# Kernel optimization log

Measured on AMD Instinct MI355X. Metric: run time of the kernel, lower is better.

The kernel has to match this reference:

```python
import math
import jax, jax.numpy as jnp
import numpy as np

B, L, C_S, C_Z, H, C, PQK, PV = 1, 768, 256, 128, 8, 32, 4, 8
OUT_DIM = H * C + H * PV * 3 + H * PV + H * 4  # 544
EPS_LN = 1e-5


def _ln(x, w, b):
    m = jnp.mean(x, axis=-1, keepdims=True)
    v = jnp.mean((x - m) ** 2, axis=-1, keepdims=True)
    return (x - m) * jax.lax.rsqrt(v + EPS_LN) * w + b


def setup_inputs() -> dict:
    key = jax.random.key(0)
    ks = jax.random.split(key, 16)
    f = lambda k, shape, s=1.0: jax.random.normal(k, shape, jnp.float32) * s
    w = 0.05  # weight init scale
    return {
        "s": f(ks[0], (B, L, C_S)),
        "z": f(ks[1], (B, L, L, C_Z)),
        "R": f(ks[2], (B, L, 3, 3)),
        "t": f(ks[3], (B, L, 3)),
        "mask": jnp.ones((B, L), jnp.float32),
        "ln_s_w": jnp.ones((C_S,), jnp.float32),
        "ln_s_b": jnp.zeros((C_S,), jnp.float32),
        "ln_z_w": jnp.ones((C_Z,), jnp.float32),
        "ln_z_b": jnp.zeros((C_Z,), jnp.float32),
        "Wq": f(ks[4], (C_S, H * C), w),
        "Wk": f(ks[5], (C_S, H * C), w),
        "Wv": f(ks[6], (C_S, H * C), w),
        "W_pair_bias": f(ks[7], (C_Z, H), w),
        "Wq_pts": f(ks[8], (C_S, H * PQK * 3), w),
        "Wk_pts": f(ks[9], (C_S, H * PQK * 3), w),
        "Wv_pts": f(ks[10], (C_S, H * PV * 3), w),
        "point_weights": f(ks[11], (H,), 0.1),
        "W_pair_out": f(ks[12], (C_Z, H * 4), w),
        "W_out": f(ks[13], (OUT_DIM, C_S), w),
        "b_out": jnp.zeros((C_S,), jnp.float32),
    }


def reference(s, z, R, t, mask, ln_s_w, ln_s_b, ln_z_w, ln_z_b,
              Wq, Wk, Wv, W_pair_bias, Wq_pts, Wk_pts, Wv_pts,
              point_weights, W_pair_out, W_out, b_out):
    s = _ln(s, ln_s_w, ln_s_b)               # [B,L,c_s]
    z = _ln(z, ln_z_w, ln_z_b)               # [B,L,L,c_z]

    q = (s @ Wq).reshape(B, L, H, C)
    k = (s @ Wk).reshape(B, L, H, C)
    v = (s @ Wv).reshape(B, L, H, C)

    scalar_logits = jnp.einsum('bihc,bjhc->bhij', q, k) / math.sqrt(C)
    pair_bias = jnp.transpose(z @ W_pair_bias, (0, 3, 1, 2))  # [B,H,L,L]

    q_pts = (s @ Wq_pts).reshape(B, L, H, PQK, 3)
    k_pts = (s @ Wk_pts).reshape(B, L, H, PQK, 3)
    v_pts = (s @ Wv_pts).reshape(B, L, H, PV, 3)

    t_b = t[:, :, None, None, :]
    apply_T = lambda p: jnp.einsum('blxy,blhpy->blhpx', R, p) + t_b
    q_pts_g = apply_T(q_pts)  # [B,L,H,Pqk,3]
    k_pts_g = apply_T(k_pts)
    v_pts_g = apply_T(v_pts)  # [B,L,H,Pv,3]

    diff = q_pts_g[:, :, None] - k_pts_g[:, None]          # [B,L,L,H,P,3]
    sq_dist = jnp.sum(diff ** 2, axis=(-1, -2))            # [B,L,L,H]
    sq_dist = jnp.transpose(sq_dist, (0, 3, 1, 2))         # [B,H,L,L]

    pw = jax.nn.softplus(point_weights)[None, :, None, None]
    logits = scalar_logits + pair_bias - 0.5 * pw * sq_dist

    pair_mask = mask[:, :, None] * mask[:, None, :]
    logits = jnp.where(pair_mask[:, None] == 0, -1e9, logits)
    attn = jax.nn.softmax(logits, axis=-1)                 # [B,H,L,L]

    scalar_out = jnp.einsum('bhij,bjhc->bihc', attn, v).reshape(B, L, H * C)

    pair_v = (z @ W_pair_out).reshape(B, L, L, H, 4)
    pair_out = jnp.einsum('bhij,bijhd->bihd', attn, pair_v).reshape(B, L, H * 4)

    pt_out_g = jnp.einsum('bhij,bjhpc->bihpc', attn, v_pts_g)    # [B,L,H,Pv,3]
    # invert transform: R^T (x - t)
    pt_out_l = jnp.einsum('blxy,blhpx->blhpy', R, pt_out_g - t_b)
    point_out = pt_out_l.reshape(B, L, H * PV * 3)
    point_norms = jnp.sqrt(jnp.sum(pt_out_l ** 2, axis=-1) + 1e-8).reshape(B, L, H * PV)

    s_update = jnp.concatenate([scalar_out, point_out, point_norms, pair_out], axis=-1)
    s_update = s_update @ W_out + b_out
    s_update = s_update * mask[:, :, None]
    return s_update, attn
```

## Files before the change

kernel.cpp:

```cpp
#include <hip/hip_runtime.h>
#include <math.h>

#define L 768
#define CS 256
#define CZ 128
#define H 8
#define LL (L*L)

typedef __attribute__((ext_vector_type(8))) short bf16x8;
typedef __attribute__((ext_vector_type(4))) float floatx4;

static __device__ __forceinline__ unsigned short f2bf(float f){
  unsigned int u = __float_as_uint(f);
  unsigned int r = (u + 0x7fffu + ((u >> 16) & 1u)) >> 16;
  return (unsigned short)r;
}
static __device__ __forceinline__ float bf2f(unsigned short u){
  return __uint_as_float(((unsigned int)u) << 16);
}

__global__ void k_ln_s(const float* __restrict__ s, const float* __restrict__ w,
                       const float* __restrict__ b, float* __restrict__ out) {
  int i = blockIdx.x, t = threadIdx.x;
  __shared__ float red[256];
  float x = s[i*CS + t];
  red[t] = x; __syncthreads();
  for (int s2=128; s2>0; s2>>=1){ if (t<s2) red[t]+=red[t+s2]; __syncthreads(); }
  float mean = red[0] * (1.0f/CS); __syncthreads();
  float d = x - mean;
  red[t] = d*d; __syncthreads();
  for (int s2=128; s2>0; s2>>=1){ if (t<s2) red[t]+=red[t+s2]; __syncthreads(); }
  float var = red[0] * (1.0f/CS);
  float rstd = rsqrtf(var + 1e-5f);
  out[i*CS+t] = d*rstd*w[t] + b[t];
}

__global__ void k_proj(const float* __restrict__ s_n,
                       const float* __restrict__ Wq, const float* __restrict__ Wk, const float* __restrict__ Wv,
                       const float* __restrict__ Wqp, const float* __restrict__ Wkp, const float* __restrict__ Wvp,
                       const float* __restrict__ R, const float* __restrict__ t,
                       float* __restrict__ q, float* __restrict__ kT, float* __restrict__ v,
                       float* __restrict__ qpg, float* __restrict__ kpgT, float* __restrict__ vpg) {
  int i0 = blockIdx.x*2, tid = threadIdx.x;
  __shared__ float srow[2][256];
  __shared__ float qraw[2][96], kraw[2][96], vraw[2][192];
  __shared__ float Rl[2][9], tl[2][3];
  srow[0][tid] = s_n[i0*CS + tid];
  srow[1][tid] = s_n[(i0+1)*CS + tid];
  if (tid < 18) Rl[tid/9][tid%9] = R[i0*9 + tid];
  if (tid >= 24 && tid < 30) tl[(tid-24)/3][(tid-24)%3] = t[i0*3 + (tid-24)];
  __syncthreads();
  float aq0=0.f, ak0=0.f, av0=0.f, aq1=0.f, ak1=0.f, av1=0.f;
  #pragma unroll 4
  for (int c=0;c<256;c++){
    float s0=srow[0][c], s1=srow[1][c];
    float wq=Wq[c*256+tid], wk=Wk[c*256+tid], wv=Wv[c*256+tid];
    aq0=fmaf(s0,wq,aq0); aq1=fmaf(s1,wq,aq1);
    ak0=fmaf(s0,wk,ak0); ak1=fmaf(s1,wk,ak1);
    av0=fmaf(s0,wv,av0); av1=fmaf(s1,wv,av1);
  }
  q[i0*256+tid]=aq0; q[(i0+1)*256+tid]=aq1;
  kT[(size_t)tid*L + i0]=ak0; kT[(size_t)tid*L + i0+1]=ak1;
  v[i0*256+tid]=av0; v[(i0+1)*256+tid]=av1;
  if (tid < 96){
    float a10=0.f,a20=0.f,a11=0.f,a21=0.f;
    #pragma unroll 4
    for (int c=0;c<256;c++){
      float s0=srow[0][c], s1=srow[1][c];
      float w1=Wqp[c*96+tid], w2=Wkp[c*96+tid];
      a10=fmaf(s0,w1,a10); a11=fmaf(s1,w1,a11);
      a20=fmaf(s0,w2,a20); a21=fmaf(s1,w2,a21);
    }
    qraw[0][tid]=a10; qraw[1][tid]=a11; kraw[0][tid]=a20; kraw[1][tid]=a21;
  }
  if (tid < 192){
    float a30=0.f,a31=0.f;
    #pragma unroll 4
    for (int c=0;c<256;c++){
      float w3=Wvp[c*192+tid];
      a30=fmaf(srow[0][c],w3,a30); a31=fmaf(srow[1][c],w3,a31);
    }
    vraw[0][tid]=a30; vraw[1][tid]=a31;
  }
  __syncthreads();
  #pragma unroll
  for (int rr=0; rr<2; rr++){
    int i = i0 + rr;
    if (tid < 32){
      int b0 = tid*3;
      float px=qraw[rr][b0], py=qraw[rr][b0+1], pz=qraw[rr][b0+2];
      #pragma unroll
      for (int x=0;x<3;x++)
        qpg[i*96 + b0 + x] = Rl[rr][x*3]*px + Rl[rr][x*3+1]*py + Rl[rr][x*3+2]*pz + tl[rr][x];
    } else if (tid < 64){
      int b0 = (tid-32)*3;
      float px=kraw[rr][b0], py=kraw[rr][b0+1], pz=kraw[rr][b0+2];
      #pragma unroll
      for (int x=0;x<3;x++)
        kpgT[(size_t)(b0+x)*L + i] = Rl[rr][x*3]*px + Rl[rr][x*3+1]*py + Rl[rr][x*3+2]*pz + tl[rr][x];
    } else if (tid < 128){
      int b0 = (tid-64)*3;
      float px=vraw[rr][b0], py=vraw[rr][b0+1], pz=vraw[rr][b0+2];
      #pragma unroll
      for (int x=0;x<3;x++)
        vpg[i*192 + b0 + x] = Rl[rr][x*3]*px + Rl[rr][x*3+1]*py + Rl[rr][x*3+2]*pz + tl[rr][x];
    }
  }
}

__global__ void k_prep(const float* __restrict__ lzw, const float* __restrict__ lzb,
                       const float* __restrict__ Wpb, const float* __restrict__ Wpo,
                       unsigned short* __restrict__ Bpack, float* __restrict__ uv) {
  int tid = threadIdx.x, bx = blockIdx.x;
  if (bx == 0){
    if (tid < 48){
      int o = tid;
      float uo = 0.f, vo = 0.f;
      for (int c=0;c<128;c++){
        float W = (o<8) ? Wpb[c*8+o] : ((o<40) ? Wpo[c*32+o-8] : 0.f);
        uo = fmaf(lzw[c], W, uo);
        vo = fmaf(lzb[c], W, vo);
      }
      uv[o] = uo; uv[48+o] = vo;
    }
    return;
  }
  int idx = (bx-1)*256 + tid;
  int jj = idx & 7, lane = (idx>>3)&63, kb = (idx>>9)&3, nt = idx>>11;
  int c = kb*32 + (lane>>4)*8 + jj;
  int o = nt*16 + (lane&15);
  float W = (o<8) ? Wpb[c*8+o] : ((o<40) ? Wpo[c*32+o-8] : 0.f);
  Bpack[idx] = f2bf(lzw[c]*W);
}

__global__ __launch_bounds__(256) void k_zfuse(
    const float* __restrict__ z, const unsigned short* __restrict__ Bpack,
    const float* __restrict__ uv, float* __restrict__ pb, unsigned short* __restrict__ pvb) {
  int i = blockIdx.x, jt = blockIdx.y, tid = threadIdx.x;
  int j0 = jt * 128;
  __shared__ unsigned short znb[128*136];
  __shared__ float smean[128], srstd[128];

  int lane = tid & 63;
  const bf16x8* Bp = (const bf16x8*)Bpack;
  bf16x8 bfr[3][4];
  #pragma unroll
  for (int nt=0; nt<3; nt++)
    #pragma unroll
    for (int kb=0; kb<4; kb++)
      bfr[nt][kb] = Bp[(nt*4+kb)*64 + lane];

  int row = tid >> 1, sub = tid & 1;
  const float4* zrow = (const float4*)(z + ((size_t)i*L + j0 + row)*CZ);
  float sm = 0.f, sq = 0.f;
  #pragma unroll 8
  for (int kk=0; kk<16; kk++){
    float4 v4 = zrow[sub + 2*kk];
    sm += (v4.x+v4.y)+(v4.z+v4.w);
    sq = fmaf(v4.x,v4.x, fmaf(v4.y,v4.y, fmaf(v4.z,v4.z, fmaf(v4.w,v4.w, sq))));
    ushort4 pk = make_ushort4(f2bf(v4.x), f2bf(v4.y), f2bf(v4.z), f2bf(v4.w));
    *(ushort4*)&znb[row*136 + (sub+2*kk)*4] = pk;
  }
  sm += __shfl_xor(sm,1); sq += __shfl_xor(sq,1);
  if (sub == 0){
    float mean = sm*(1.f/128.f);
    float var  = sq*(1.f/128.f) - mean*mean;
    smean[row] = mean; srstd[row] = rsqrtf(var + 1e-5f);
  }

  int w = tid >> 6;
  int n16 = lane & 15, quad = lane >> 4;
  #pragma unroll
  for (int mt2=0; mt2<2; mt2++){
    int mt = w*2 + mt2;
    floatx4 acc0 = {0,0,0,0}, acc1 = {0,0,0,0}, acc2 = {0,0,0,0};
    #pragma unroll
    for (int kb=0; kb<4; kb++){
      bf16x8 afrag = *(const bf16x8*)&znb[(mt*16 + n16)*136 + kb*32 + quad*8];
      acc0 = __builtin_amdgcn_mfma_f32_16x16x32_bf16(afrag, bfr[0][kb], acc0, 0,0,0);
      acc1 = __builtin_amdgcn_mfma_f32_16x16x32_bf16(afrag, bfr[1][kb], acc1, 0,0,0);
      acc2 = __builtin_amdgcn_mfma_f32_16x16x32_bf16(afrag, bfr[2][kb], acc2, 0,0,0);
    }
    #pragma unroll
    for (int nt=0; nt<3; nt++){
      int o = nt*16 + n16;
      if (o >= 40) continue;
      float uo = uv[o], vo = uv[48+o];
      const floatx4 acc = (nt==0) ? acc0 : (nt==1) ? acc1 : acc2;
      #pragma unroll
      for (int reg=0; reg<4; reg++){
        int jl = mt*16 + quad*4 + reg;
        int j = j0 + jl;
        float val = srstd[jl]*(acc[reg] - smean[jl]*uo) + vo;
        if (o < 8) pb[(size_t)o*LL + (size_t)i*L + j] = val;
        else {
          int oo = o - 8;
          pvb[(size_t)(oo>>2)*LL*4 + ((size_t)i*L + j)*4 + (oo&3)] = f2bf(val);
        }
      }
    }
  }
}

__global__ __launch_bounds__(256) void k_attn3(
    const float* __restrict__ q, const float* __restrict__ kT, const float* __restrict__ v,
    const float* __restrict__ qpg, const float* __restrict__ kpgT, const float* __restrict__ vpg,
    float* __restrict__ attn, const unsigned short* __restrict__ pvb,
    const float* __restrict__ R, const float* __restrict__ t,
    const float* __restrict__ point_weights, const float* __restrict__ mask,
    float* __restrict__ su) {
  const int h   = blockIdx.y;
  const int tid = threadIdx.x;
  const int il  = tid >> 5;
  const int i   = blockIdx.x*8 + il;
  const int jg  = tid & 31;

  __shared__ float sml[8][768];
  __shared__ float sptg[8][24];
  __shared__ float sptl[8][24];

  const float pw = log1pf(__expf(point_weights[h]));
  const float mi = mask[i];

  float qreg[32];
  {
    const float4* qr = (const float4*)(q + (size_t)i*256 + h*32);
    #pragma unroll
    for (int c4=0;c4<8;c4++){
      float4 t4 = qr[c4];
      qreg[c4*4+0]=t4.x; qreg[c4*4+1]=t4.y; qreg[c4*4+2]=t4.z; qreg[c4*4+3]=t4.w;
    }
  }
  float qp[12];
  {
    const float4* qr = (const float4*)(qpg + (size_t)i*96 + h*12);
    #pragma unroll
    for (int c4=0;c4<3;c4++){
      float4 t4 = qr[c4];
      qp[c4*4+0]=t4.x; qp[c4*4+1]=t4.y; qp[c4*4+2]=t4.z; qp[c4*4+3]=t4.w;
    }
  }

  const float* kbase  = kT   + (size_t)(h*32)*L + jg*4;
  const float* kpbase = kpgT + (size_t)(h*12)*L + jg*4;
  float* pbrow = attn + (size_t)h*LL + (size_t)i*L + jg*4;

  float lgr[24];
  #pragma unroll
  for (int jt=0; jt<6; jt++){
    const int j0 = jt*128;
    float d0=0.f,d1=0.f,d2=0.f,d3=0.f;
    #pragma unroll
    for (int c=0;c<32;c++){
      float4 kv = *(const float4*)(kbase + (size_t)c*L + j0);
      float qc = qreg[c];
      d0 = fmaf(qc, kv.x, d0); d1 = fmaf(qc, kv.y, d1);
      d2 = fmaf(qc, kv.z, d2); d3 = fmaf(qc, kv.w, d3);
    }
    float s0=0.f,s1=0.f,s2=0.f,s3=0.f;
    #pragma unroll
    for (int pc=0;pc<12;pc++){
      float4 kv = *(const float4*)(kpbase + (size_t)pc*L + j0);
      float qc = qp[pc];
      float e0=qc-kv.x, e1=qc-kv.y, e2=qc-kv.z, e3=qc-kv.w;
      s0=fmaf(e0,e0,s0); s1=fmaf(e1,e1,s1); s2=fmaf(e2,e2,s2); s3=fmaf(e3,e3,s3);
    }
    float4 pb4 = *(const float4*)(pbrow + j0);
    float4 mk4 = *(const float4*)(mask + j0 + jg*4);
    const float SCL = 0.17677669529663687f;
    float l0 = fmaf(d0,SCL,pb4.x) - 0.5f*pw*s0;
    float l1 = fmaf(d1,SCL,pb4.y) - 0.5f*pw*s1;
    float l2 = fmaf(d2,SCL,pb4.z) - 0.5f*pw*s2;
    float l3 = fmaf(d3,SCL,pb4.w) - 0.5f*pw*s3;
    if (mi*mk4.x == 0.f) l0 = -1e9f;
    if (mi*mk4.y == 0.f) l1 = -1e9f;
    if (mi*mk4.z == 0.f) l2 = -1e9f;
    if (mi*mk4.w == 0.f) l3 = -1e9f;
    lgr[jt*4+0]=l0; lgr[jt*4+1]=l1; lgr[jt*4+2]=l2; lgr[jt*4+3]=l3;
  }

  float m = -1e30f;
  #pragma unroll
  for (int u=0;u<24;u++) m = fmaxf(m, lgr[u]);
  #pragma unroll
  for (int d=1; d<32; d<<=1) m = fmaxf(m, __shfl_xor(m, d));
  float ss = 0.f;
  #pragma unroll
  for (int u=0;u<24;u++){ float e = __expf(lgr[u]-m); lgr[u]=e; ss+=e; }
  #pragma unroll
  for (int d=1; d<32; d<<=1) ss += __shfl_xor(ss, d);
  float inv = 1.0f/ss;
  #pragma unroll
  for (int u=0;u<24;u++) lgr[u] *= inv;
  #pragma unroll
  for (int jt=0;jt<6;jt++){
    float4 a4;
    a4.x=lgr[jt*4+0]; a4.y=lgr[jt*4+1]; a4.z=lgr[jt*4+2]; a4.w=lgr[jt*4+3];
    *(float4*)&sml[il][jt*128 + jg*4] = a4;
    *(float4*)(pbrow + jt*128) = a4;
  }
  __syncthreads();

  {
    const float* vp = v + h*32 + jg;
    const float* aw = sml[il];
    float a0=0.f,a1=0.f,a2=0.f,a3=0.f;
    for (int j=0;j<768;j+=4){
      float4 w4 = *(const float4*)&aw[j];
      a0 = fmaf(w4.x, vp[(j+0)*256], a0);
      a1 = fmaf(w4.y, vp[(j+1)*256], a1);
      a2 = fmaf(w4.z, vp[(j+2)*256], a2);
      a3 = fmaf(w4.w, vp[(j+3)*256], a3);
    }
    su[(size_t)i*544 + h*32 + jg] = (a0+a1)+(a2+a3);
  }

  if (tid < 192){
    int i2 = tid/24, e = tid - i2*24;
    const float* pp = vpg + h*24 + e;
    const float* aw = sml[i2];
    float a0=0.f,a1=0.f,a2=0.f,a3=0.f;
    for (int j=0;j<768;j+=4){
      float4 w4 = *(const float4*)&aw[j];
      a0 = fmaf(w4.x, pp[(j+0)*192], a0);
      a1 = fmaf(w4.y, pp[(j+1)*192], a1);
      a2 = fmaf(w4.z, pp[(j+2)*192], a2);
      a3 = fmaf(w4.w, pp[(j+3)*192], a3);
    }
    sptg[i2][e] = (a0+a1)+(a2+a3);
  } else if (tid < 224){
    int qq = tid-192; int i2 = qq>>2, d = qq&3;
    int ii = blockIdx.x*8 + i2;
    const unsigned short* bp = pvb + (size_t)h*LL*4 + (size_t)ii*L*4 + d;
    const float* aw = sml[i2];
    float a0=0.f,a1=0.f,a2=0.f,a3=0.f;
    for (int j=0;j<768;j+=4){
      float4 w4 = *(const float4*)&aw[j];
      a0 = fmaf(w4.x, bf2f(bp[(j+0)*4]), a0);
      a1 = fmaf(w4.y, bf2f(bp[(j+1)*4]), a1);
      a2 = fmaf(w4.z, bf2f(bp[(j+2)*4]), a2);
      a3 = fmaf(w4.w, bf2f(bp[(j+3)*4]), a3);
    }
    su[(size_t)ii*544 + 512 + h*4 + d] = (a0+a1)+(a2+a3);
  }
  __syncthreads();

  if (tid < 192){
    int i2 = tid/24, rem = tid - i2*24, p = rem/3, y = rem - p*3;
    int ii = blockIdx.x*8 + i2;
    float acc = 0.f;
    #pragma unroll
    for (int x=0;x<3;x++)
      acc = fmaf(R[ii*9 + x*3 + y], sptg[i2][p*3+x] - t[ii*3+x], acc);
    sptl[i2][rem] = acc;
    su[(size_t)ii*544 + 256 + h*24 + rem] = acc;
  }
  __syncthreads();

  if (tid < 64){
    int i2 = tid>>3, p = tid&7;
    int ii = blockIdx.x*8 + i2;
    float x0=sptl[i2][p*3], x1=sptl[i2][p*3+1], x2=sptl[i2][p*3+2];
    su[(size_t)ii*544 + 448 + h*8 + p] = sqrtf(x0*x0+x1*x1+x2*x2 + 1e-8f);
  }
}

__global__ void k_out(const float* __restrict__ su_pre, const float* __restrict__ W_out,
                      const float* __restrict__ b_out, const float* __restrict__ mask,
                      float* __restrict__ out) {
  int i = blockIdx.x, tid = threadIdx.x;
  __shared__ float srow[544];
  for (int idx=tid; idx<544; idx+=256) srow[idx] = su_pre[i*544+idx];
  __syncthreads();
  float acc = b_out[tid];
  #pragma unroll 4
  for (int c=0;c<544;c++) acc = fmaf(srow[c], W_out[c*256+tid], acc);
  out[i*256+tid] = acc * mask[i];
}

extern "C" void kernel_launch(void* const* d_in, const int* in_sizes, int n_in,
                              void* d_out, int out_size, void* d_ws, size_t ws_size,
                              hipStream_t stream) {
  const float* s    = (const float*)d_in[0];
  const float* z    = (const float*)d_in[1];
  const float* R    = (const float*)d_in[2];
  const float* t    = (const float*)d_in[3];
  const float* mask = (const float*)d_in[4];
  const float* lsw  = (const float*)d_in[5];
  const float* lsb  = (const float*)d_in[6];
  const float* lzw  = (const float*)d_in[7];
  const float* lzb  = (const float*)d_in[8];
  const float* Wq   = (const float*)d_in[9];
  const float* Wk   = (const float*)d_in[10];
  const float* Wv   = (const float*)d_in[11];
  const float* Wpb  = (const float*)d_in[12];
  const float* Wqp  = (const float*)d_in[13];
  const float* Wkp  = (const float*)d_in[14];
  const float* Wvp  = (const float*)d_in[15];
  const float* pwts = (const float*)d_in[16];
  const float* Wpo  = (const float*)d_in[17];
  const float* Wout = (const float*)d_in[18];
  const float* bout = (const float*)d_in[19];

  float* out0 = (float*)d_out;
  float* attn = out0 + (size_t)L*CS;

  float* ws   = (float*)d_ws;
  float* s_n  = ws;                        size_t off = (size_t)L*CS;
  float* q    = ws + off;                  off += (size_t)L*CS;
  float* kT   = ws + off;                  off += (size_t)L*CS;
  float* v    = ws + off;                  off += (size_t)L*CS;
  float* qpg  = ws + off;                  off += (size_t)L*96;
  float* kpgT = ws + off;                  off += (size_t)L*96;
  float* vpg  = ws + off;                  off += (size_t)L*192;
  unsigned short* pvb = (unsigned short*)(ws + off); off += (size_t)LL*16;
  float* su   = ws + off;                  off += (size_t)L*544;
  unsigned short* Bpack = (unsigned short*)(ws + off); off += 3072;
  float* uv   = ws + off;                  off += 96;

  k_prep<<<25, 256, 0, stream>>>(lzw, lzb, Wpb, Wpo, Bpack, uv);
  k_ln_s<<<L, 256, 0, stream>>>(s, lsw, lsb, s_n);
  k_proj<<<L/2, 256, 0, stream>>>(s_n, Wq, Wk, Wv, Wqp, Wkp, Wvp, R, t,
                                  q, kT, v, qpg, kpgT, vpg);
  k_zfuse<<<dim3(L, L/128), 256, 0, stream>>>(z, Bpack, uv, attn, pvb);
  k_attn3<<<dim3(L/8, H), 256, 0, stream>>>(q, kT, v, qpg, kpgT, vpg, attn, pvb,
                                            R, t, pwts, mask, su);
  k_out<<<L, 256, 0, stream>>>(su, Wout, bout, mask, out0);
}
```

Before: 790.1 us.

## Split attention into logits/softmax kernel and separate attn@V kernel with register tiling

The fused attention kernel is split in two. The first computes logits and the softmax, writes attn, and folds the pair-value reduction into registers with a warp shuffle while the probabilities are still live. It drops the shared-memory staging and declares a higher occupancy bound. The second kernel reloads attn rows into shared memory and computes the scalar and point value products, with each thread covering 8 query rows over a slice of keys so every loaded v element is reused 8 times, then reduces the partial sums across slices. In exchange, the attn matrix is read back from global memory and there is one more launch.

Result: slower. 880.0 us (+11.4%).

```diff
diff --git a/kernel.cpp b/kernel.cpp
--- a/kernel.cpp
+++ b/kernel.cpp
@@ -202,22 +202,16 @@
   }
 }
 
-__global__ __launch_bounds__(256) void k_attn3(
-    const float* __restrict__ q, const float* __restrict__ kT, const float* __restrict__ v,
-    const float* __restrict__ qpg, const float* __restrict__ kpgT, const float* __restrict__ vpg,
+__global__ __launch_bounds__(256, 4) void k_logits(
+    const float* __restrict__ q, const float* __restrict__ kT,
+    const float* __restrict__ qpg, const float* __restrict__ kpgT,
     float* __restrict__ attn, const unsigned short* __restrict__ pvb,
-    const float* __restrict__ R, const float* __restrict__ t,
     const float* __restrict__ point_weights, const float* __restrict__ mask,
     float* __restrict__ su) {
-  const int h   = blockIdx.y;
-  const int tid = threadIdx.x;
-  const int il  = tid >> 5;
-  const int i   = blockIdx.x*8 + il;
-  const int jg  = tid & 31;
-
-  __shared__ float sml[8][768];
-  __shared__ float sptg[8][24];
-  __shared__ float sptl[8][24];
+  const int h  = blockIdx.y;
+  const int il = threadIdx.x >> 5;
+  const int i  = blockIdx.x*8 + il;
+  const int jg = threadIdx.x & 31;
 
   const float pw = log1pf(__expf(point_weights[h]));
   const float mi = mask[i];
@@ -296,72 +290,152 @@
   for (int jt=0;jt<6;jt++){
     float4 a4;
     a4.x=lgr[jt*4+0]; a4.y=lgr[jt*4+1]; a4.z=lgr[jt*4+2]; a4.w=lgr[jt*4+3];
-    *(float4*)&sml[il][jt*128 + jg*4] = a4;
     *(float4*)(pbrow + jt*128) = a4;
   }
+
+  float pq0=0.f,pq1=0.f,pq2=0.f,pq3=0.f;
+  const unsigned short* pvrow = pvb + (size_t)h*LL*4 + (size_t)i*L*4 + (size_t)jg*16;
+  #pragma unroll
+  for (int jt=0;jt<6;jt++){
+    #pragma unroll
+    for (int r=0;r<4;r++){
+      ushort4 pk = *(const ushort4*)(pvrow + jt*512 + r*4);
+      float a = lgr[jt*4+r];
+      pq0 = fmaf(a, bf2f(pk.x), pq0);
+      pq1 = fmaf(a, bf2f(pk.y), pq1);
+      pq2 = fmaf(a, bf2f(pk.z), pq2);
+      pq3 = fmaf(a, bf2f(pk.w), pq3);
+    }
+  }
+  #pragma unroll
+  for (int d=1; d<32; d<<=1){
+    pq0 += __shfl_xor(pq0,d); pq1 += __shfl_xor(pq1,d);
+    pq2 += __shfl_xor(pq2,d); pq3 += __shfl_xor(pq3,d);
+  }
+  if (jg == 0){
+    float* so = su + (size_t)i*544 + 512 + h*4;
+    so[0]=pq0; so[1]=pq1; so[2]=pq2; so[3]=pq3;
+  }
+}
+
+__global__ __launch_bounds__(256) void k_pv(
+    const float* __restrict__ attn, const float* __restrict__ v,
+    const float* __restrict__ vpg, const float* __restrict__ R,
+    const float* __restrict__ t, float* __restrict__ su) {
+  const int h = blockIdx.y, i0 = blockIdx.x*8, tid = threadIdx.x;
+  __shared__ float awt[8][768];
+  __shared__ float pf[8][8][32];
+  __shared__ float sptg[8][24];
+  __shared__ float sptl[8][24];
+
+  const float* ab = attn + (size_t)h*LL + (size_t)i0*L;
+  float* awl = &awt[0][0];
+  #pragma unroll
+  for (int w2=0; w2<6; w2++){
+    float4 t4 = *(const float4*)(ab + (size_t)(w2*256+tid)*4);
+    *(float4*)(awl + (w2*256+tid)*4) = t4;
+  }
   __syncthreads();
 
   {
-    const float* vp = v + h*32 + jg;
-    const float* aw = sml[il];
-    float a0=0.f,a1=0.f,a2=0.f,a3=0.f;
-    for (int j=0;j<768;j+=4){
-      float4 w4 = *(const float4*)&aw[j];
-      a0 = fmaf(w4.x, vp[(j+0)*256], a0);
-      a1 = fmaf(w4.y, vp[(j+1)*256], a1);
-      a2 = fmaf(w4.z, vp[(j+2)*256], a2);
-      a3 = fmaf(w4.w, vp[(j+3)*256], a3);
-    }
-    su[(size_t)i*544 + h*32 + jg] = (a0+a1)+(a2+a3);
-  }
+    const int c = tid & 31, p = tid >> 5;
+    const float* vb = v + h*32 + c;
+    float ac0=0.f,ac1=0.f,ac2=0.f,ac3=0.f,ac4=0.f,ac5=0.f,ac6=0.f,ac7=0.f;
+    const int jb = p*96;
+    #pragma unroll 4
+    for (int s=0; s<24; s++){
+      const int j = jb + s*4;
+      float v0 = vb[(size_t)(j+0)*256];
+      float v1 = vb[(size_t)(j+1)*256];
+      float v2 = vb[(size_t)(j+2)*256];
+      float v3 = vb[(size_t)(j+3)*256];
+      float4 a0 = *(const float4*)&awt[0][j];
+      float4 a1 = *(const float4*)&awt[1][j];
+      float4 a2 = *(const float4*)&awt[2][j];
+      float4 a3 = *(const float4*)&awt[3][j];
+      float4 a4 = *(const float4*)&awt[4][j];
+      float4 a5 = *(const float4*)&awt[5][j];
+      float4 a6 = *(const float4*)&awt[6][j];
+      float4 a7 = *(const float4*)&awt[7][j];
+      ac0 = fmaf(a0.x,v0, fmaf(a0.y,v1, fmaf(a0.z,v2, fmaf(a0.w,v3, ac0))));
+      ac1 = fmaf(a1.x,v0, fmaf(a1.y,v1, fmaf(a1.z,v2, fmaf(a1.w,v3, ac1))));
+      ac2 = fmaf(a2.x,v0, fmaf(a2.y,v1, fmaf(a2.z,v2, fmaf(a2.w,v3, ac2))));
+      ac3 = fmaf(a3.x,v0, fmaf(a3.y,v1, fmaf(a3.z,v2, fmaf(a3.w,v3, ac3))));
+      ac4 = fmaf(a4.x,v0, fmaf(a4.y,v1, fmaf(a4.z,v2, fmaf(a4.w,v3, ac4))));
+      ac5 = fmaf(a5.x,v0, fmaf(a5.y,v1, fmaf(a5.z,v2, fmaf(a5.w,v3, ac5))));
+      ac6 = fmaf(a6.x,v0, fmaf(a6.y,v1, fmaf(a6.z,v2, fmaf(a6.w,v3, ac6))));
+      ac7 = fmaf(a7.x,v0, fmaf(a7.y,v1, fmaf(a7.z,v2, fmaf(a7.w,v3, ac7))));
+    }
+    pf[p][0][c]=ac0; pf[p][1][c]=ac1; pf[p][2][c]=ac2; pf[p][3][c]=ac3;
+    pf[p][4][c]=ac4; pf[p][5][c]=ac5; pf[p][6][c]=ac6; pf[p][7][c]=ac7;
+  }
+  __syncthreads();
+  {
+    const int ii = tid >> 5, c = tid & 31;
+    float a = 0.f;
+    #pragma unroll
+    for (int p=0;p<8;p++) a += pf[p][ii][c];
+    su[(size_t)(i0+ii)*544 + h*32 + c] = a;
+  }
+  __syncthreads();
 
   if (tid < 192){
-    int i2 = tid/24, e = tid - i2*24;
-    const float* pp = vpg + h*24 + e;
-    const float* aw = sml[i2];
-    float a0=0.f,a1=0.f,a2=0.f,a3=0.f;
-    for (int j=0;j<768;j+=4){
-      float4 w4 = *(const float4*)&aw[j];
-      a0 = fmaf(w4.x, pp[(j+0)*192], a0);
-      a1 = fmaf(w4.y, pp[(j+1)*192], a1);
-      a2 = fmaf(w4.z, pp[(j+2)*192], a2);
-      a3 = fmaf(w4.w, pp[(j+3)*192], a3);
-    }
-    sptg[i2][e] = (a0+a1)+(a2+a3);
-  } else if (tid < 224){
-    int qq = tid-192; int i2 = qq>>2, d = qq&3;
-    int ii = blockIdx.x*8 + i2;
-    const unsigned short* bp = pvb + (size_t)h*LL*4 + (size_t)ii*L*4 + d;
-    const float* aw = sml[i2];
-    float a0=0.f,a1=0.f,a2=0.f,a3=0.f;
-    for (int j=0;j<768;j+=4){
-      float4 w4 = *(const float4*)&aw[j];
-      a0 = fmaf(w4.x, bf2f(bp[(j+0)*4]), a0);
-      a1 = fmaf(w4.y, bf2f(bp[(j+1)*4]), a1);
-      a2 = fmaf(w4.z, bf2f(bp[(j+2)*4]), a2);
-      a3 = fmaf(w4.w, bf2f(bp[(j+3)*4]), a3);
-    }
-    su[(size_t)ii*544 + 512 + h*4 + d] = (a0+a1)+(a2+a3);
-  }
-  __syncthreads();
-
+    const int c = tid % 24, p = tid / 24;
+    const float* pb2 = vpg + h*24 + c;
+    float ac0=0.f,ac1=0.f,ac2=0.f,ac3=0.f,ac4=0.f,ac5=0.f,ac6=0.f,ac7=0.f;
+    const int jb = p*96;
+    #pragma unroll 4
+    for (int s=0; s<24; s++){
+      const int j = jb + s*4;
+      float v0 = pb2[(size_t)(j+0)*192];
+      float v1 = pb2[(size_t)(j+1)*192];
+      float v2 = pb2[(size_t)(j+2)*192];
+      float v3 = pb2[(size_t)(j+3)*192];
+      float4 a0 = *(const float4*)&awt[0][j];
+      float4 a1 = *(const float4*)&awt[1][j];
+      float4 a2 = *(const float4*)&awt[2][j];
+      float4 a3 = *(const float4*)&awt[3][j];
+      float4 a4 = *(const float4*)&awt[4][j];
+      float4 a5 = *(const float4*)&awt[5][j];
+      float4 a6 = *(const float4*)&awt[6][j];
+      float4 a7 = *(const float4*)&awt[7][j];
+      ac0 = fmaf(a0.x,v0, fmaf(a0.y,v1, fmaf(a0.z,v2, fmaf(a0.w,v3, ac0))));
+      ac1 = fmaf(a1.x,v0, fmaf(a1.y,v1, fmaf(a1.z,v2, fmaf(a1.w,v3, ac1))));
+      ac2 = fmaf(a2.x,v0, fmaf(a2.y,v1, fmaf(a2.z,v2, fmaf(a2.w,v3, ac2))));
+      ac3 = fmaf(a3.x,v0, fmaf(a3.y,v1, fmaf(a3.z,v2, fmaf(a3.w,v3, ac3))));
+      ac4 = fmaf(a4.x,v0, fmaf(a4.y,v1, fmaf(a4.z,v2, fmaf(a4.w,v3, ac4))));
+      ac5 = fmaf(a5.x,v0, fmaf(a5.y,v1, fmaf(a5.z,v2, fmaf(a5.w,v3, ac5))));
+      ac6 = fmaf(a6.x,v0, fmaf(a6.y,v1, fmaf(a6.z,v2, fmaf(a6.w,v3, ac6))));
+      ac7 = fmaf(a7.x,v0, fmaf(a7.y,v1, fmaf(a7.z,v2, fmaf(a7.w,v3, ac7))));
+    }
+    pf[p][0][c]=ac0; pf[p][1][c]=ac1; pf[p][2][c]=ac2; pf[p][3][c]=ac3;
+    pf[p][4][c]=ac4; pf[p][5][c]=ac5; pf[p][6][c]=ac6; pf[p][7][c]=ac7;
+  }
+  __syncthreads();
   if (tid < 192){
-    int i2 = tid/24, rem = tid - i2*24, p = rem/3, y = rem - p*3;
-    int ii = blockIdx.x*8 + i2;
+    const int ii = tid / 24, e = tid % 24;
+    float a = 0.f;
+    #pragma unroll
+    for (int p=0;p<8;p++) a += pf[p][ii][e];
+    sptg[ii][e] = a;
+  }
+  __syncthreads();
+  if (tid < 192){
+    const int ii = tid/24, rem = tid%24, pp = rem/3, y = rem - pp*3;
+    const int gi = i0 + ii;
     float acc = 0.f;
     #pragma unroll
     for (int x=0;x<3;x++)
-      acc = fmaf(R[ii*9 + x*3 + y], sptg[i2][p*3+x] - t[ii*3+x], acc);
-    sptl[i2][rem] = acc;
-    su[(size_t)ii*544 + 256 + h*24 + rem] = acc;
-  }
-  __syncthreads();
-
+      acc = fmaf(R[gi*9 + x*3 + y], sptg[ii][pp*3+x] - t[gi*3+x], acc);
+    sptl[ii][rem] = acc;
+    su[(size_t)gi*544 + 256 + h*24 + rem] = acc;
+  }
+  __syncthreads();
   if (tid < 64){
-    int i2 = tid>>3, p = tid&7;
-    int ii = blockIdx.x*8 + i2;
-    float x0=sptl[i2][p*3], x1=sptl[i2][p*3+1], x2=sptl[i2][p*3+2];
-    su[(size_t)ii*544 + 448 + h*8 + p] = sqrtf(x0*x0+x1*x1+x2*x2 + 1e-8f);
+    const int ii = tid>>3, pp = tid&7;
+    const int gi = i0 + ii;
+    float x0=sptl[ii][pp*3], x1=sptl[ii][pp*3+1], x2=sptl[ii][pp*3+2];
+    su[(size_t)gi*544 + 448 + h*8 + pp] = sqrtf(x0*x0+x1*x1+x2*x2 + 1e-8f);
   }
 }
 
@@ -423,7 +497,8 @@
   k_proj<<<L/2, 256, 0, stream>>>(s_n, Wq, Wk, Wv, Wqp, Wkp, Wvp, R, t,
                                   q, kT, v, qpg, kpgT, vpg);
   k_zfuse<<<dim3(L, L/128), 256, 0, stream>>>(z, Bpack, uv, attn, pvb);
-  k_attn3<<<dim3(L/8, H), 256, 0, stream>>>(q, kT, v, qpg, kpgT, vpg, attn, pvb,
-                                            R, t, pwts, mask, su);
+  k_logits<<<dim3(L/8, H), 256, 0, stream>>>(q, kT, qpg, kpgT, attn, pvb,
+                                             pwts, mask, su);
+  k_pv<<<dim3(L/8, H), 256, 0, stream>>>(attn, v, vpg, R, t, su);
   k_out<<<L, 256, 0, stream>>>(su, Wout, bout, mask, out0);
 }
```
